# Optimization experiments

Hardware: AMD Instinct MI355X
Metric: run time of the kernel (lower is better)

The kernel has to match this reference:

```python
import jax, jax.numpy as jnp
import numpy as np

B, S, E, H = 2, 2048, 1024, 16
HD = E // H            # 64
LAMBDA_INIT = 0.8
EPS = 1e-6


def setup_inputs() -> dict:
    key = jax.random.key(0)
    ks = jax.random.split(key, 8)
    return {
        "x": jax.random.normal(ks[0], (B, S, E), dtype=jnp.float32),
        "w_qkv": jax.random.normal(ks[1], (E, 3 * E), dtype=jnp.float32) * (E ** -0.5),
        "wo": jax.random.normal(ks[2], (E, E), dtype=jnp.float32) * (E ** -0.5),
        "lambda_q1": jax.random.normal(ks[3], (HD,), dtype=jnp.float32) * 0.1,
        "lambda_q2": jax.random.normal(ks[4], (HD,), dtype=jnp.float32) * 0.1,
        "lambda_k1": jax.random.normal(ks[5], (HD,), dtype=jnp.float32) * 0.1,
        "lambda_k2": jax.random.normal(ks[6], (HD,), dtype=jnp.float32) * 0.1,
        "norm_w": jnp.ones((H, HD), dtype=jnp.float32),
    }


def reference(x, w_qkv, wo, lambda_q1, lambda_q2, lambda_k1, lambda_k2, norm_w):
    b, s, e = x.shape
    qkv = x @ w_qkv                                   # [b, s, 3e]
    q, k, v = jnp.split(qkv, 3, axis=-1)
    def to_heads(t):
        return t.reshape(b, s, H, HD).transpose(0, 2, 1, 3)  # [b, H, s, hd]
    q, k, v = to_heads(q), to_heads(k), to_heads(v)
    q1, q2 = jnp.split(q, 2, axis=-1)                 # [b, H, s, hd/2]
    k1, k2 = jnp.split(k, 2, axis=-1)
    scale = 1.0 / jnp.sqrt(jnp.asarray(HD, dtype=x.dtype))  # note: full head_dim, as in source
    a1 = jax.nn.softmax(jnp.einsum('bhsd,bhtd->bhst', q1, k1) * scale, axis=-1)
    a2 = jax.nn.softmax(jnp.einsum('bhsd,bhtd->bhst', q2, k2) * scale, axis=-1)
    lam = jnp.exp(jnp.dot(lambda_q1, lambda_k1)) - jnp.exp(jnp.dot(lambda_q2, lambda_k2)) + LAMBDA_INIT
    a = a1 - lam * a2                                 # [b, H, s, s]
    out = jnp.einsum('bhst,bhtd->bhsd', a, v)         # [b, H, s, hd]
    # per-head RMSNorm, scaled by (1 - lambda_init)
    rms = jnp.sqrt(jnp.mean(out * out, axis=-1, keepdims=True) + EPS)
    out_n = (out / rms) * norm_w[None, :, None, :] * (1.0 - LAMBDA_INIT)
    # replicate source's cat(dim=1) -> transpose(1,2) -> view(b, s, e)
    out_cat = out_n.reshape(b, H * s, HD)             # concat of per-head [b, s, hd]
    out_final = out_cat.transpose(0, 2, 1).reshape(b, s, e)
    return out_final @ wo
```

## Files before the change

### kernel.cpp

```cpp
#include <hip/hip_runtime.h>
#include <math.h>

#define B_ 2
#define S_ 2048
#define E_ 1024
#define H_ 16
#define HD_ 64
#define LAMBDA_INIT 0.8f
#define EPS_ 1e-6f

typedef __attribute__((ext_vector_type(8))) short short8;
typedef __attribute__((ext_vector_type(4))) float floatx4;
typedef __attribute__((ext_vector_type(16))) float floatx16;

__device__ __forceinline__ unsigned short f2bf(float f) {
  unsigned u = __float_as_uint(f);
  u += 0x7FFFu + ((u >> 16) & 1u);
  return (unsigned short)(u >> 16);
}

__device__ __forceinline__ void gl_lds16(const void* g, void* l) {
  __builtin_amdgcn_global_load_lds((const __attribute__((address_space(1))) void*)g,
                                   (__attribute__((address_space(3))) void*)l,
                                   16, 0, 0);
}

__global__ __launch_bounds__(256) void cast_bf16(const float* __restrict__ in,
                                                 unsigned short* __restrict__ out,
                                                 int n4) {
  for (int i = blockIdx.x * 256 + threadIdx.x; i < n4; i += gridDim.x * 256) {
    float4 v = ((const float4*)in)[i];
    ushort4 w;
    w.x = f2bf(v.x); w.y = f2bf(v.y); w.z = f2bf(v.z); w.w = f2bf(v.w);
    ((ushort4*)out)[i] = w;
  }
}

__global__ __launch_bounds__(256) void transpose_cast(const float* __restrict__ in,
                                                      unsigned short* __restrict__ out,
                                                      int R, int C) {
  __shared__ float tile[64][65];
  const int tid = threadIdx.x;
  const int c0 = blockIdx.x * 64;
  const int r0 = blockIdx.y * 64;
#pragma unroll
  for (int it = 0; it < 16; it++) {
    int e = tid + it * 256;
    int rr = e >> 6, cc = e & 63;
    tile[rr][cc] = in[(size_t)(r0 + rr) * C + c0 + cc];
  }
  __syncthreads();
#pragma unroll
  for (int it = 0; it < 16; it++) {
    int e = tid + it * 256;
    int rr = e >> 6, cc = e & 63;
    out[(size_t)(c0 + rr) * R + r0 + cc] = f2bf(tile[cc][rr]);
  }
}

template <bool BF16OUT, int BNT>
__global__ __launch_bounds__(256, BNT == 64 ? 2 : 1) void gemm_bt(
    const unsigned short* __restrict__ A, const unsigned short* __restrict__ Bt,
    void* __restrict__ C, int M, int N, int K) {
  __shared__ __align__(16) unsigned short As[128 * 64];
  __shared__ __align__(16) unsigned short Bs[BNT * 64];
  const int tid = threadIdx.x;
  const int wave = tid >> 6, lane = tid & 63;
  const int lane15 = lane & 15, quad = lane >> 4;
  const int m0 = blockIdx.y * 128;
  const int n0 = blockIdx.x * BNT;
  const int wm = (wave & 1) * 64, wn = (wave >> 1) * (BNT / 2);
  const int NI = BNT / 32;

  floatx4 acc[4][NI];
#pragma unroll
  for (int mi = 0; mi < 4; mi++)
#pragma unroll
    for (int ni = 0; ni < NI; ni++) acc[mi][ni] = (floatx4)0.0f;

  const int rsA = wave * 32 + (lane >> 3);
  const int rsB = wave * (BNT / 4) + (lane >> 3);
  const int cph = lane & 7;

  for (int k0 = 0; k0 < K; k0 += 64) {
    __syncthreads();
#pragma unroll
    for (int j = 0; j < 4; j++) {
      int r = rsA + j * 8;
      int cl = cph ^ (r & 7);
      gl_lds16(A + (size_t)(m0 + r) * K + k0 + cl * 8, &As[(wave * 32 + j * 8) * 64]);
    }
#pragma unroll
    for (int j = 0; j < BNT / 32; j++) {
      int r = rsB + j * 8;
      int cl = cph ^ (r & 7);
      gl_lds16(Bt + (size_t)(n0 + r) * K + k0 + cl * 8,
               &Bs[(wave * (BNT / 4) + j * 8) * 64]);
    }
    __syncthreads();

#pragma unroll
    for (int ks = 0; ks < 2; ks++) {
      short8 af[4], bf[NI];
#pragma unroll
      for (int mi = 0; mi < 4; mi++) {
        int r = wm + mi * 16 + lane15;
        int phys = (ks * 4 + quad) ^ (r & 7);
        af[mi] = *(const short8*)(&As[r * 64 + phys * 8]);
      }
#pragma unroll
      for (int ni = 0; ni < NI; ni++) {
        int r = wn + ni * 16 + lane15;
        int phys = (ks * 4 + quad) ^ (r & 7);
        bf[ni] = *(const short8*)(&Bs[r * 64 + phys * 8]);
      }
#pragma unroll
      for (int mi = 0; mi < 4; mi++)
#pragma unroll
        for (int ni = 0; ni < NI; ni++)
          acc[mi][ni] = __builtin_amdgcn_mfma_f32_16x16x32_bf16(af[mi], bf[ni],
                                                                acc[mi][ni], 0, 0, 0);
    }
  }

#pragma unroll
  for (int mi = 0; mi < 4; mi++)
#pragma unroll
    for (int ni = 0; ni < NI; ni++)
#pragma unroll
      for (int reg = 0; reg < 4; reg++) {
        int row = m0 + wm + mi * 16 + quad * 4 + reg;
        int col = n0 + wn + ni * 16 + lane15;
        float v = acc[mi][ni][reg];
        if (BF16OUT)
          ((unsigned short*)C)[(size_t)row * N + col] = f2bf(v);
        else
          ((float*)C)[(size_t)row * N + col] = v;
      }
}

__global__ __launch_bounds__(256) void flash_attn_mfma(
    const unsigned short* __restrict__ qkB, const unsigned short* __restrict__ vTB,
    const float* __restrict__ lq1, const float* __restrict__ lq2,
    const float* __restrict__ lk1, const float* __restrict__ lk2,
    const float* __restrict__ norm_w, float* __restrict__ out_n) {
  __shared__ __align__(16) unsigned short Ks[2][64 * 64];
  __shared__ __align__(16) unsigned short Vs[2][64 * 64];

  const int tid = threadIdx.x;
  const int wave = tid >> 6, lane = tid & 63;
  const int l31 = lane & 31, hi = lane >> 5;

  const int bid = (blockIdx.x & 7) * 64 + (blockIdx.x >> 3);
  const int qt = bid & 15;
  const int h = (bid >> 4) & 15;
  const int b = bid >> 8;
  const int q0 = qt * 128;

  float a1 = 0.f, a2 = 0.f;
  for (int d = 0; d < HD_; d++) {
    a1 += lq1[d] * lk1[d];
    a2 += lq2[d] * lk2[d];
  }
  const float lam = __expf(a1) - __expf(a2) + LAMBDA_INIT;

  short8 qf[2][2];
  {
    const unsigned short* qrow =
        qkB + (size_t)(b * S_ + q0 + wave * 32 + l31) * 2048 + h * 64;
#pragma unroll
    for (int s = 0; s < 2; s++)
#pragma unroll
      for (int cs = 0; cs < 2; cs++)
        qf[s][cs] = *(const short8*)(qrow + s * 32 + cs * 16 + hi * 8);
  }

  floatx16 accO[2][2];
#pragma unroll
  for (int s = 0; s < 2; s++)
#pragma unroll
    for (int n = 0; n < 2; n++) accO[s][n] = (floatx16)0.0f;
  float lsum[2] = {0.f, 0.f};
  const floatx16 zero16 = (floatx16)0.0f;

  const int srow = tid >> 3;
  const int scol = tid & 7;
  const size_t kgbase = (size_t)(b * S_) * 2048 + 1024 + h * 64;
  const size_t vgbase = (size_t)h * 64 * 4096 + b * 2048;

#pragma unroll
  for (int rnd = 0; rnd < 2; rnd++) {
    int r = rnd * 32 + srow;
    int cl = scol ^ (r & 7);
    gl_lds16(qkB + kgbase + (size_t)r * 2048 + cl * 8,
             &Ks[0][(rnd * 32 + wave * 8) * 64]);
    gl_lds16(vTB + vgbase + (size_t)r * 4096 + cl * 8,
             &Vs[0][(rnd * 32 + wave * 8) * 64]);
  }
  __syncthreads();

  int cur = 0;
  for (int t = 0; t < S_ / 64; t++) {
    if (t < S_ / 64 - 1) {
      const size_t kg = kgbase + (size_t)(t + 1) * 64 * 2048;
      const size_t vg = vgbase + (size_t)(t + 1) * 64;
#pragma unroll
      for (int rnd = 0; rnd < 2; rnd++) {
        int r = rnd * 32 + srow;
        int cl = scol ^ (r & 7);
        gl_lds16(qkB + kg + (size_t)r * 2048 + cl * 8,
                 &Ks[cur ^ 1][(rnd * 32 + wave * 8) * 64]);
        gl_lds16(vTB + vg + (size_t)r * 4096 + cl * 8,
                 &Vs[cur ^ 1][(rnd * 32 + wave * 8) * 64]);
      }
    }
    const unsigned short* Kc = Ks[cur];
    const unsigned short* Vc = Vs[cur];

#pragma unroll
    for (int kb = 0; kb < 2; kb++) {
      const int krow = kb * 32 + l31;
      const int kx = krow & 7;
      short8 pf[2][2];
#pragma unroll
      for (int s = 0; s < 2; s++) {
        floatx16 accS = zero16;
#pragma unroll
        for (int cs = 0; cs < 2; cs++) {
          const int pc = (s * 4 + cs * 2 + hi) ^ kx;
          const short8 kf = *(const short8*)(Kc + krow * 64 + pc * 8);
          accS = __builtin_amdgcn_mfma_f32_32x32x16_bf16(kf, qf[s][cs], accS, 0, 0, 0);
        }
        unsigned w[8];
        float ls = 0.f;
#pragma unroll
        for (int i = 0; i < 8; i++) {
          float p0 = __expf(accS[2 * i] * 0.125f);
          float p1 = __expf(accS[2 * i + 1] * 0.125f);
          ls += p0 + p1;
          asm("v_cvt_pk_bf16_f32 %0, %1, %2" : "=v"(w[i]) : "v"(p0), "v"(p1));
        }
        lsum[s] += ls;
        asm volatile("v_permlane32_swap_b32 %0, %1" : "+v"(w[0]), "+v"(w[2]));
        asm volatile("v_permlane32_swap_b32 %0, %1" : "+v"(w[1]), "+v"(w[3]));
        asm volatile("v_permlane32_swap_b32 %0, %1" : "+v"(w[4]), "+v"(w[6]));
        asm volatile("v_permlane32_swap_b32 %0, %1" : "+v"(w[5]), "+v"(w[7]));
        uint4 u0 = make_uint4(w[0], w[1], w[2], w[3]);
        uint4 u1 = make_uint4(w[4], w[5], w[6], w[7]);
        pf[s][0] = __builtin_bit_cast(short8, u0);
        pf[s][1] = __builtin_bit_cast(short8, u1);
      }
#pragma unroll
      for (int ks2 = 0; ks2 < 2; ks2++)
#pragma unroll
        for (int n = 0; n < 2; n++) {
          const int vrow = n * 32 + l31;
          const int pc = (kb * 4 + ks2 * 2 + hi) ^ (vrow & 7);
          const short8 vf = *(const short8*)(Vc + vrow * 64 + pc * 8);
          accO[0][n] = __builtin_amdgcn_mfma_f32_32x32x16_bf16(pf[0][ks2], vf,
                                                               accO[0][n], 0, 0, 0);
          accO[1][n] = __builtin_amdgcn_mfma_f32_32x32x16_bf16(pf[1][ks2], vf,
                                                               accO[1][n], 0, 0, 0);
        }
    }
    __syncthreads();
    cur ^= 1;
  }

  lsum[0] += __shfl_xor(lsum[0], 32, 64);
  lsum[1] += __shfl_xor(lsum[1], 32, 64);
  const float* nw = norm_w + h * HD_;
  const float nw0 = nw[l31], nw1 = nw[32 + l31];
#pragma unroll
  for (int r = 0; r < 16; r++) {
    const int qr = (r & 3) + 8 * (r >> 2) + 4 * hi;
    const float s1 = __shfl(lsum[0], qr, 64);
    const float s2 = __shfl(lsum[1], qr, 64);
    const float inv1 = 1.0f / s1;
    const float c2 = lam / s2;
    float o0 = accO[0][0][r] * inv1 - accO[1][0][r] * c2;
    float o1 = accO[0][1][r] * inv1 - accO[1][1][r] * c2;
    float ss = o0 * o0 + o1 * o1;
#pragma unroll
    for (int msk = 1; msk <= 16; msk <<= 1) ss += __shfl_xor(ss, msk, 64);
    const float rsc = (1.0f - LAMBDA_INIT) * rsqrtf(ss * (1.0f / 64.0f) + EPS_);
    float* dst = out_n + ((size_t)(b * H_ + h) * S_ + q0 + wave * 32 + qr) * HD_;
    dst[l31] = o0 * rsc * nw0;
    dst[32 + l31] = o1 * rsc * nw1;
  }
}

__global__ __launch_bounds__(256) void reshape_out(const float* __restrict__ out_n,
                                                   unsigned short* __restrict__ hidden) {
  __shared__ float tile[64][65];
  const int tid = threadIdx.x;
  const int bi = blockIdx.x;
  const int tb = bi & 31;
  const int h = (bi >> 5) & 15;
  const int b = bi >> 9;
  const int t0 = tb * 64;
  const float* src = out_n + (((size_t)b * H_ + h) * S_ + t0) * HD_;
#pragma unroll
  for (int rr = 0; rr < 16; rr++) {
    int e = tid + rr * 256;
    tile[e >> 6][e & 63] = src[e];
  }
  __syncthreads();
  unsigned short* dst = hidden + (size_t)b * (S_ * E_) + h * S_ + t0;
#pragma unroll
  for (int rr = 0; rr < 16; rr++) {
    int e = tid + rr * 256;
    int d = e >> 6, tt = e & 63;
    dst[(size_t)d * (H_ * S_) + tt] = f2bf(tile[tt][d]);
  }
}

extern "C" void kernel_launch(void* const* d_in, const int* in_sizes, int n_in,
                              void* d_out, int out_size, void* d_ws, size_t ws_size,
                              hipStream_t stream) {
  const float* x = (const float*)d_in[0];
  const float* w_qkv = (const float*)d_in[1];
  const float* wo = (const float*)d_in[2];
  const float* lq1 = (const float*)d_in[3];
  const float* lq2 = (const float*)d_in[4];
  const float* lk1 = (const float*)d_in[5];
  const float* lk2 = (const float*)d_in[6];
  const float* norm_w = (const float*)d_in[7];
  float* out = (float*)d_out;

  unsigned short* xB = (unsigned short*)d_ws;
  unsigned short* WT = xB + (size_t)4096 * 1024;
  unsigned short* woT = WT + (size_t)3072 * 1024;
  unsigned short* qkB = woT + (size_t)1024 * 1024;
  unsigned short* vTB = qkB + (size_t)4096 * 2048;
  unsigned short* hidB = vTB + (size_t)1024 * 4096;
  float* out_n = (float*)(hidB + (size_t)4096 * 1024);

  cast_bf16<<<1024, 256, 0, stream>>>(x, xB, 4096 * 1024 / 4);
  transpose_cast<<<dim3(48, 16), 256, 0, stream>>>(w_qkv, WT, 1024, 3072);
  transpose_cast<<<dim3(16, 16), 256, 0, stream>>>(wo, woT, 1024, 1024);

  gemm_bt<true, 128><<<dim3(2048 / 128, 4096 / 128), 256, 0, stream>>>(
      xB, WT, (void*)qkB, 4096, 2048, 1024);
  gemm_bt<true, 64><<<dim3(4096 / 64, 1024 / 128), 256, 0, stream>>>(
      WT + (size_t)2048 * 1024, xB, (void*)vTB, 1024, 4096, 1024);

  flash_attn_mfma<<<B_ * H_ * (S_ / 128), 256, 0, stream>>>(qkB, vTB, lq1, lq2, lk1,
                                                            lk2, norm_w, out_n);
  reshape_out<<<B_ * H_ * (S_ / 64), 256, 0, stream>>>(out_n, hidB);
  gemm_bt<false, 64><<<dim3(1024 / 64, 4096 / 128), 256, 0, stream>>>(
      hidB, woT, (void*)out, 4096, 1024, 1024);
}
```

Before: 251.8 us.

## Split differential attention halves across separate waves with 512-thread blocks

The attention kernel now runs 8 waves per block instead of 4. Each pair of waves shares one 32-row query slice, and each wave of the pair handles one of the two q/k halves (softmax branches), so per-wave accumulators and register pressure drop by half. Each thread now stages one K and one V row per tile instead of two. At the end, the second-half wave passes its output accumulators and row sums through LDS, reusing the KV buffer, so the first wave can combine them with lambda and apply the RMSNorm. This raises occupancy and parallelism, at the cost of an extra LDS exchange and a block-wide barrier in the epilogue.

Result: faster. 236.4 us (-6.1%).

```diff
diff --git a/kernel.cpp b/kernel.cpp
--- a/kernel.cpp
+++ b/kernel.cpp
@@ -139,17 +139,18 @@
       }
 }
 
-__global__ __launch_bounds__(256) void flash_attn_mfma(
+__global__ __launch_bounds__(512, 4) void flash_attn_mfma(
     const unsigned short* __restrict__ qkB, const unsigned short* __restrict__ vTB,
     const float* __restrict__ lq1, const float* __restrict__ lq2,
     const float* __restrict__ lk1, const float* __restrict__ lk2,
     const float* __restrict__ norm_w, float* __restrict__ out_n) {
-  __shared__ __align__(16) unsigned short Ks[2][64 * 64];
-  __shared__ __align__(16) unsigned short Vs[2][64 * 64];
+  __shared__ __align__(16) unsigned short KV[2][2][64 * 64];
+  __shared__ float Lex[4][64];
 
   const int tid = threadIdx.x;
   const int wave = tid >> 6, lane = tid & 63;
   const int l31 = lane & 31, hi = lane >> 5;
+  const int qsub = wave >> 1, sw = wave & 1;
 
   const int bid = (blockIdx.x & 7) * 64 + (blockIdx.x >> 3);
   const int qt = bid & 15;
@@ -164,23 +165,19 @@
   }
   const float lam = __expf(a1) - __expf(a2) + LAMBDA_INIT;
 
-  short8 qf[2][2];
+  short8 qf[2];
   {
     const unsigned short* qrow =
-        qkB + (size_t)(b * S_ + q0 + wave * 32 + l31) * 2048 + h * 64;
-#pragma unroll
-    for (int s = 0; s < 2; s++)
-#pragma unroll
-      for (int cs = 0; cs < 2; cs++)
-        qf[s][cs] = *(const short8*)(qrow + s * 32 + cs * 16 + hi * 8);
-  }
-
-  floatx16 accO[2][2];
-#pragma unroll
-  for (int s = 0; s < 2; s++)
-#pragma unroll
-    for (int n = 0; n < 2; n++) accO[s][n] = (floatx16)0.0f;
-  float lsum[2] = {0.f, 0.f};
+        qkB + (size_t)(b * S_ + q0 + qsub * 32 + l31) * 2048 + h * 64 + sw * 32;
+#pragma unroll
+    for (int cs = 0; cs < 2; cs++)
+      qf[cs] = *(const short8*)(qrow + cs * 16 + hi * 8);
+  }
+
+  floatx16 accO[2];
+#pragma unroll
+  for (int n = 0; n < 2; n++) accO[n] = (floatx16)0.0f;
+  float lsum = 0.f;
   const floatx16 zero16 = (floatx16)0.0f;
 
   const int srow = tid >> 3;
@@ -188,105 +185,108 @@
   const size_t kgbase = (size_t)(b * S_) * 2048 + 1024 + h * 64;
   const size_t vgbase = (size_t)h * 64 * 4096 + b * 2048;
 
-#pragma unroll
-  for (int rnd = 0; rnd < 2; rnd++) {
-    int r = rnd * 32 + srow;
-    int cl = scol ^ (r & 7);
-    gl_lds16(qkB + kgbase + (size_t)r * 2048 + cl * 8,
-             &Ks[0][(rnd * 32 + wave * 8) * 64]);
-    gl_lds16(vTB + vgbase + (size_t)r * 4096 + cl * 8,
-             &Vs[0][(rnd * 32 + wave * 8) * 64]);
-  }
+#define STAGE(t_, buf_)                                                        \
+  {                                                                            \
+    const size_t kg_ = kgbase + (size_t)(t_) * 64 * 2048;                      \
+    const size_t vg_ = vgbase + (size_t)(t_) * 64;                             \
+    const int cl_ = scol ^ (srow & 7);                                         \
+    gl_lds16(qkB + kg_ + (size_t)srow * 2048 + cl_ * 8,                        \
+             &KV[buf_][0][(wave * 8) * 64]);                                   \
+    gl_lds16(vTB + vg_ + (size_t)srow * 4096 + cl_ * 8,                        \
+             &KV[buf_][1][(wave * 8) * 64]);                                   \
+  }
+
+  STAGE(0, 0);
   __syncthreads();
 
   int cur = 0;
   for (int t = 0; t < S_ / 64; t++) {
-    if (t < S_ / 64 - 1) {
-      const size_t kg = kgbase + (size_t)(t + 1) * 64 * 2048;
-      const size_t vg = vgbase + (size_t)(t + 1) * 64;
-#pragma unroll
-      for (int rnd = 0; rnd < 2; rnd++) {
-        int r = rnd * 32 + srow;
-        int cl = scol ^ (r & 7);
-        gl_lds16(qkB + kg + (size_t)r * 2048 + cl * 8,
-                 &Ks[cur ^ 1][(rnd * 32 + wave * 8) * 64]);
-        gl_lds16(vTB + vg + (size_t)r * 4096 + cl * 8,
-                 &Vs[cur ^ 1][(rnd * 32 + wave * 8) * 64]);
-      }
-    }
-    const unsigned short* Kc = Ks[cur];
-    const unsigned short* Vc = Vs[cur];
+    if (t < S_ / 64 - 1) STAGE(t + 1, cur ^ 1);
+    const unsigned short* Kc = &KV[cur][0][0];
+    const unsigned short* Vc = &KV[cur][1][0];
 
 #pragma unroll
     for (int kb = 0; kb < 2; kb++) {
       const int krow = kb * 32 + l31;
       const int kx = krow & 7;
-      short8 pf[2][2];
-#pragma unroll
-      for (int s = 0; s < 2; s++) {
-        floatx16 accS = zero16;
-#pragma unroll
-        for (int cs = 0; cs < 2; cs++) {
-          const int pc = (s * 4 + cs * 2 + hi) ^ kx;
-          const short8 kf = *(const short8*)(Kc + krow * 64 + pc * 8);
-          accS = __builtin_amdgcn_mfma_f32_32x32x16_bf16(kf, qf[s][cs], accS, 0, 0, 0);
-        }
-        unsigned w[8];
-        float ls = 0.f;
-#pragma unroll
-        for (int i = 0; i < 8; i++) {
-          float p0 = __expf(accS[2 * i] * 0.125f);
-          float p1 = __expf(accS[2 * i + 1] * 0.125f);
-          ls += p0 + p1;
-          asm("v_cvt_pk_bf16_f32 %0, %1, %2" : "=v"(w[i]) : "v"(p0), "v"(p1));
-        }
-        lsum[s] += ls;
-        asm volatile("v_permlane32_swap_b32 %0, %1" : "+v"(w[0]), "+v"(w[2]));
-        asm volatile("v_permlane32_swap_b32 %0, %1" : "+v"(w[1]), "+v"(w[3]));
-        asm volatile("v_permlane32_swap_b32 %0, %1" : "+v"(w[4]), "+v"(w[6]));
-        asm volatile("v_permlane32_swap_b32 %0, %1" : "+v"(w[5]), "+v"(w[7]));
-        uint4 u0 = make_uint4(w[0], w[1], w[2], w[3]);
-        uint4 u1 = make_uint4(w[4], w[5], w[6], w[7]);
-        pf[s][0] = __builtin_bit_cast(short8, u0);
-        pf[s][1] = __builtin_bit_cast(short8, u1);
-      }
-#pragma unroll
-      for (int ks2 = 0; ks2 < 2; ks2++)
+      floatx16 accS = zero16;
+#pragma unroll
+      for (int cs = 0; cs < 2; cs++) {
+        const int pc = (sw * 4 + cs * 2 + hi) ^ kx;
+        const short8 kf = *(const short8*)(Kc + krow * 64 + pc * 8);
+        accS = __builtin_amdgcn_mfma_f32_32x32x16_bf16(kf, qf[cs], accS, 0, 0, 0);
+      }
+      unsigned w[8];
+      float ls = 0.f;
+#pragma unroll
+      for (int i = 0; i < 8; i++) {
+        float p0 = __expf(accS[2 * i] * 0.125f);
+        float p1 = __expf(accS[2 * i + 1] * 0.125f);
+        ls += p0 + p1;
+        asm("v_cvt_pk_bf16_f32 %0, %1, %2" : "=v"(w[i]) : "v"(p0), "v"(p1));
+      }
+      lsum += ls;
+      asm volatile("v_permlane32_swap_b32 %0, %1" : "+v"(w[0]), "+v"(w[2]));
+      asm volatile("v_permlane32_swap_b32 %0, %1" : "+v"(w[1]), "+v"(w[3]));
+      asm volatile("v_permlane32_swap_b32 %0, %1" : "+v"(w[4]), "+v"(w[6]));
+      asm volatile("v_permlane32_swap_b32 %0, %1" : "+v"(w[5]), "+v"(w[7]));
+      uint4 u0 = make_uint4(w[0], w[1], w[2], w[3]);
+      uint4 u1 = make_uint4(w[4], w[5], w[6], w[7]);
+      short8 pf0 = __builtin_bit_cast(short8, u0);
+      short8 pf1 = __builtin_bit_cast(short8, u1);
+#pragma unroll
+      for (int ks2 = 0; ks2 < 2; ks2++) {
+        const short8 pa = ks2 ? pf1 : pf0;
 #pragma unroll
         for (int n = 0; n < 2; n++) {
           const int vrow = n * 32 + l31;
           const int pc = (kb * 4 + ks2 * 2 + hi) ^ (vrow & 7);
           const short8 vf = *(const short8*)(Vc + vrow * 64 + pc * 8);
-          accO[0][n] = __builtin_amdgcn_mfma_f32_32x32x16_bf16(pf[0][ks2], vf,
-                                                               accO[0][n], 0, 0, 0);
-          accO[1][n] = __builtin_amdgcn_mfma_f32_32x32x16_bf16(pf[1][ks2], vf,
-                                                               accO[1][n], 0, 0, 0);
+          accO[n] = __builtin_amdgcn_mfma_f32_32x32x16_bf16(pa, vf, accO[n], 0, 0, 0);
         }
+      }
     }
     __syncthreads();
     cur ^= 1;
   }
-
-  lsum[0] += __shfl_xor(lsum[0], 32, 64);
-  lsum[1] += __shfl_xor(lsum[1], 32, 64);
-  const float* nw = norm_w + h * HD_;
-  const float nw0 = nw[l31], nw1 = nw[32 + l31];
-#pragma unroll
-  for (int r = 0; r < 16; r++) {
-    const int qr = (r & 3) + 8 * (r >> 2) + 4 * hi;
-    const float s1 = __shfl(lsum[0], qr, 64);
-    const float s2 = __shfl(lsum[1], qr, 64);
-    const float inv1 = 1.0f / s1;
-    const float c2 = lam / s2;
-    float o0 = accO[0][0][r] * inv1 - accO[1][0][r] * c2;
-    float o1 = accO[0][1][r] * inv1 - accO[1][1][r] * c2;
-    float ss = o0 * o0 + o1 * o1;
-#pragma unroll
-    for (int msk = 1; msk <= 16; msk <<= 1) ss += __shfl_xor(ss, msk, 64);
-    const float rsc = (1.0f - LAMBDA_INIT) * rsqrtf(ss * (1.0f / 64.0f) + EPS_);
-    float* dst = out_n + ((size_t)(b * H_ + h) * S_ + q0 + wave * 32 + qr) * HD_;
-    dst[l31] = o0 * rsc * nw0;
-    dst[32 + l31] = o1 * rsc * nw1;
+#undef STAGE
+
+  lsum += __shfl_xor(lsum, 32, 64);
+
+  float* LF = (float*)&KV[0][0][0];
+  if (sw == 1) {
+    Lex[qsub][lane] = lsum;
+#pragma unroll
+    for (int n = 0; n < 2; n++)
+#pragma unroll
+      for (int r = 0; r < 16; r++)
+        LF[qsub * 2048 + (n * 16 + r) * 64 + lane] = accO[n][r];
+  }
+  __syncthreads();
+
+  if (sw == 0) {
+    const float ls2v = Lex[qsub][lane];
+    const float* nw = norm_w + h * HD_;
+    const float nw0 = nw[l31], nw1 = nw[32 + l31];
+#pragma unroll
+    for (int r = 0; r < 16; r++) {
+      const int qr = (r & 3) + 8 * (r >> 2) + 4 * hi;
+      const float s1 = __shfl(lsum, qr, 64);
+      const float s2 = __shfl(ls2v, qr, 64);
+      const float inv1 = 1.0f / s1;
+      const float c2 = lam / s2;
+      const float b0 = LF[qsub * 2048 + (0 * 16 + r) * 64 + lane];
+      const float b1 = LF[qsub * 2048 + (1 * 16 + r) * 64 + lane];
+      float o0 = accO[0][r] * inv1 - b0 * c2;
+      float o1 = accO[1][r] * inv1 - b1 * c2;
+      float ss = o0 * o0 + o1 * o1;
+#pragma unroll
+      for (int msk = 1; msk <= 16; msk <<= 1) ss += __shfl_xor(ss, msk, 64);
+      const float rsc = (1.0f - LAMBDA_INIT) * rsqrtf(ss * (1.0f / 64.0f) + EPS_);
+      float* dst = out_n + ((size_t)(b * H_ + h) * S_ + q0 + qsub * 32 + qr) * HD_;
+      dst[l31] = o0 * rsc * nw0;
+      dst[32 + l31] = o1 * rsc * nw1;
+    }
   }
 }
 
@@ -345,7 +345,7 @@
   gemm_bt<true, 64><<<dim3(4096 / 64, 1024 / 128), 256, 0, stream>>>(
       WT + (size_t)2048 * 1024, xB, (void*)vTB, 1024, 4096, 1024);
 
-  flash_attn_mfma<<<B_ * H_ * (S_ / 128), 256, 0, stream>>>(qkB, vTB, lq1, lq2, lk1,
+  flash_attn_mfma<<<B_ * H_ * (S_ / 128), 512, 0, stream>>>(qkB, vTB, lq1, lq2, lk1,
                                                             lk2, norm_w, out_n);
   reshape_out<<<B_ * H_ * (S_ / 64), 256, 0, stream>>>(out_n, hidB);
   gemm_bt<false, 64><<<dim3(1024 / 64, 4096 / 128), 256, 0, stream>>>(
```
